# Performance work log

Measured on AMD Instinct MI355X. Metric: run time of the kernel, lower is better.

## Reference

```python
import jax, jax.numpy as jnp
import numpy as np

E = 8       # num experts
D = 768     # embed_dim
H = 12      # num heads
F = 3072    # expert hidden = 4*D
TOPK = 2


def setup_inputs() -> dict:
    key = jax.random.key(0)
    ks = jax.random.split(key, 8)
    B, S = 4, 1024
    s = lambda d: 1.0 / np.sqrt(d)
    return {
        "x": jax.random.normal(ks[0], (B, S, D), jnp.float32),
        "w_qkv": jax.random.normal(ks[1], (D, 3 * D), jnp.float32) * s(D),
        "b_qkv": jnp.zeros((3 * D,), jnp.float32),
        "w_o": jax.random.normal(ks[2], (D, D), jnp.float32) * s(D),
        "b_o": jnp.zeros((D,), jnp.float32),
        "w_router": jax.random.normal(ks[3], (D, E), jnp.float32) * s(D),
        "w1": jax.random.normal(ks[4], (E, D, F), jnp.float32) * s(D),
        "b1": jnp.zeros((E, F), jnp.float32),
        "w2": jax.random.normal(ks[5], (E, F, D), jnp.float32) * s(F),
        "b2": jnp.zeros((E, D), jnp.float32),
    }


def reference(x, w_qkv, b_qkv, w_o, b_o, w_router, w1, b1, w2, b2):
    B, S, Dm = x.shape
    hd = Dm // H
    # --- multi-head self-attention ---
    qkv = x @ w_qkv + b_qkv                                  # [B,S,3D]
    q, k, v = jnp.split(qkv, 3, axis=-1)
    resh = lambda t: t.reshape(B, S, H, hd).transpose(0, 2, 1, 3)  # [B,H,S,hd]
    q, k, v = resh(q), resh(k), resh(v)
    scores = jnp.einsum('bhqd,bhkd->bhqk', q, k) / np.sqrt(hd).astype(np.float32)
    attn = jax.nn.softmax(scores, axis=-1)
    ctx = jnp.einsum('bhqk,bhkd->bhqd', attn, v)
    ctx = ctx.transpose(0, 2, 1, 3).reshape(B, S, Dm)
    y = ctx @ w_o + b_o                                      # [B,S,D]
    # --- top-k MoE feed-forward ---
    t = y.reshape(B * S, Dm)                                 # [T,D]
    logits = t @ w_router                                    # [T,E]
    probs = jax.nn.softmax(logits, axis=-1)
    topv, topi = jax.lax.top_k(probs, TOPK)                  # [T,K]
    topw = topv / jnp.sum(topv, axis=-1, keepdims=True)      # renormalized gates
    T = t.shape[0]
    wfull = jnp.zeros_like(probs).at[jnp.arange(T)[:, None], topi].set(topw)  # [T,E]
    # dense all-expert compute, weighted combine (faithful to routed math)
    h = jax.nn.gelu(jnp.einsum('td,edf->etf', t, w1) + b1[:, None, :])  # [E,T,F]
    oe = jnp.einsum('etf,efd->etd', h, w2) + b2[:, None, :]              # [E,T,D]
    out = jnp.einsum('te,etd->td', wfull, oe).reshape(B, S, Dm)
    diagnostics = probs  # router probabilities as diagnostics
    return (out, diagnostics)
```

## Files before the change

kernel.cpp:

```cpp
#include <hip/hip_runtime.h>
#include <hip/hip_bf16.h>
#include <cstdint>
#include <cmath>

#define T_TOK 4096
#define DIM   768
#define HEADS 12
#define HD    64
#define NEXP  8
#define FDIM  3072

typedef __attribute__((ext_vector_type(8))) short short8v;
typedef __attribute__((ext_vector_type(4))) float float4v;

__device__ __forceinline__ float gelu_tanh(float x) {
  float u = 0.7978845608028654f * (x + 0.044715f * x * x * x);
  return 0.5f * x * (1.0f + tanhf(u));
}

__device__ __forceinline__ short f2bf(float x) {
  __hip_bfloat16 h = __float2bfloat16(x);
  return *reinterpret_cast<short*>(&h);
}

__device__ __forceinline__ void gld16(void* lds, const void* g) {
  __builtin_amdgcn_global_load_lds(
      (__attribute__((address_space(1))) void*)(uintptr_t)g,
      (__attribute__((address_space(3))) void*)(uint32_t)(uintptr_t)lds,
      16, 0, 0);
}

template<int TBM, int TBN, bool BFOUT>
__global__ __launch_bounds__(256) void gemm_f32(
    const float* __restrict__ A, const float* __restrict__ W,
    const float* __restrict__ bias, float* __restrict__ C,
    short* __restrict__ Cbf, int M, int N, int K)
{
  constexpr int MM = TBM / 16;
  constexpr int MN = TBN / 16;
  constexpr int AL4 = TBM / 64;
  constexpr int BL4 = TBN / 64;
  __shared__ float As[16][TBM + 4];
  __shared__ float Bs[16][TBN + 4];
  const int bm = blockIdx.y * TBM;
  const int bn = blockIdx.x * TBN;
  const int tid = threadIdx.x;
  const int tr = tid >> 4;
  const int tc = tid & 15;

  float acc[MM][MN] = {};

  for (int k0 = 0; k0 < K; k0 += 16) {
    #pragma unroll
    for (int i = 0; i < AL4; i++) {
      int fidx = tid + i * 256;
      int row = fidx >> 2, c4 = fidx & 3;
      float4 v = *(const float4*)&A[(size_t)(bm + row) * K + k0 + c4 * 4];
      As[c4 * 4 + 0][row] = v.x;
      As[c4 * 4 + 1][row] = v.y;
      As[c4 * 4 + 2][row] = v.z;
      As[c4 * 4 + 3][row] = v.w;
    }
    #pragma unroll
    for (int i = 0; i < BL4; i++) {
      int fidx = tid + i * 256;
      int kk = fidx / (TBN / 4), n4 = fidx % (TBN / 4);
      *(float4*)&Bs[kk][n4 * 4] =
          *(const float4*)&W[(size_t)(k0 + kk) * N + bn + n4 * 4];
    }
    __syncthreads();
    #pragma unroll
    for (int kk = 0; kk < 16; kk++) {
      float a[MM], b[MN];
      #pragma unroll
      for (int u4 = 0; u4 < MM / 4; u4++) {
        float4 t = *(const float4*)&As[kk][tr * MM + u4 * 4];
        a[u4*4+0]=t.x; a[u4*4+1]=t.y; a[u4*4+2]=t.z; a[u4*4+3]=t.w;
      }
      #pragma unroll
      for (int v4 = 0; v4 < MN / 4; v4++) {
        float4 t = *(const float4*)&Bs[kk][tc * MN + v4 * 4];
        b[v4*4+0]=t.x; b[v4*4+1]=t.y; b[v4*4+2]=t.z; b[v4*4+3]=t.w;
      }
      #pragma unroll
      for (int u = 0; u < MM; u++)
        #pragma unroll
        for (int v = 0; v < MN; v++)
          acc[u][v] = fmaf(a[u], b[v], acc[u][v]);
    }
    __syncthreads();
  }

  #pragma unroll
  for (int u = 0; u < MM; u++) {
    int row = bm + tr * MM + u;
    #pragma unroll
    for (int v4 = 0; v4 < MN / 4; v4++) {
      int col = bn + tc * MN + v4 * 4;
      float4 o;
      o.x = acc[u][v4*4+0] + bias[col+0];
      o.y = acc[u][v4*4+1] + bias[col+1];
      o.z = acc[u][v4*4+2] + bias[col+2];
      o.w = acc[u][v4*4+3] + bias[col+3];
      *(float4*)&C[(size_t)row * N + col] = o;
      if (BFOUT) {
        short4 s = make_short4(f2bf(o.x), f2bf(o.y), f2bf(o.z), f2bf(o.w));
        *(short4*)&Cbf[(size_t)row * N + col] = s;
      }
    }
  }
}

__global__ __launch_bounds__(256) void transpose_bf16(
    const float* __restrict__ W, short* __restrict__ WT, int K, int N)
{
  __shared__ float t[32][33];
  const size_t mat = (size_t)K * N;
  const float* Wp = W + blockIdx.z * mat;
  short* WTp = WT + blockIdx.z * mat;
  int n0 = blockIdx.x * 32, k0 = blockIdx.y * 32;
  int tx = threadIdx.x, ty = threadIdx.y;
  #pragma unroll
  for (int i = 0; i < 4; i++)
    t[ty + i * 8][tx] = Wp[(size_t)(k0 + ty + i * 8) * N + n0 + tx];
  __syncthreads();
  #pragma unroll
  for (int i = 0; i < 4; i++)
    WTp[(size_t)(n0 + ty + i * 8) * K + k0 + tx] = f2bf(t[tx][ty + i * 8]);
}

__global__ __launch_bounds__(256) void moe_up(
    const short* __restrict__ ybf, const short* __restrict__ WT,
    const float* __restrict__ bias, short* __restrict__ hbuf,
    const int* __restrict__ offsets, const int* __restrict__ perm,
    const int* __restrict__ tmap, const int* __restrict__ tilecnt)
{
  const int by = blockIdx.y;
  if (by >= tilecnt[0]) return;
  const int info  = tmap[by];
  const int e     = info >> 16;
  const int start = offsets[e];
  const int M     = offsets[e + 1] - start;
  const int bm    = (info & 0xffff) * 128;
  const int bn    = blockIdx.x * 128;

  __shared__ short As[4][128][8];
  __shared__ short Bs[4][128][8];
  __shared__ int   perm_s[128];

  const int tid  = threadIdx.x;
  const int lane = tid & 63;
  const int wave = tid >> 6;
  const int wm = wave >> 1, wn = wave & 1;
  const int lr = lane & 15;
  const int kb = lane >> 4;

  const short* WTe = WT + (size_t)e * ((size_t)FDIM * DIM);
  const float* be  = bias + (size_t)e * FDIM;

  if (tid < 128) {
    int rr = bm + tid;
    perm_s[tid] = (rr < M) ? perm[start + rr] : perm[start];
  }
  __syncthreads();

  const short* asrc0 = ybf + (size_t)perm_s[lane] * DIM + wave * 8;
  const short* asrc1 = ybf + (size_t)perm_s[64 + lane] * DIM + wave * 8;
  const short* bsrc0 = WTe + (size_t)(bn + lane) * DIM + wave * 8;
  const short* bsrc1 = WTe + (size_t)(bn + 64 + lane) * DIM + wave * 8;
  short* adst0 = &As[wave][0][0];
  short* adst1 = &As[wave][64][0];
  short* bdst0 = &Bs[wave][0][0];
  short* bdst1 = &Bs[wave][64][0];

  float4v acc[4][4] = {};

  for (int k0 = 0; k0 < DIM; k0 += 32) {
    __syncthreads();
    gld16(adst0, asrc0 + k0);
    gld16(adst1, asrc1 + k0);
    gld16(bdst0, bsrc0 + k0);
    gld16(bdst1, bsrc1 + k0);
    __syncthreads();

    short8v af[4], bfv[4];
    #pragma unroll
    for (int mi = 0; mi < 4; mi++)
      af[mi] = *(const short8v*)&As[kb][wm * 64 + mi * 16 + lr][0];
    #pragma unroll
    for (int ni = 0; ni < 4; ni++)
      bfv[ni] = *(const short8v*)&Bs[kb][wn * 64 + ni * 16 + lr][0];
    #pragma unroll
    for (int mi = 0; mi < 4; mi++)
      #pragma unroll
      for (int ni = 0; ni < 4; ni++)
        acc[mi][ni] = __builtin_amdgcn_mfma_f32_16x16x32_bf16(
            af[mi], bfv[ni], acc[mi][ni], 0, 0, 0);
  }

  #pragma unroll
  for (int ni = 0; ni < 4; ni++) {
    int col = bn + wn * 64 + ni * 16 + lr;
    float b = be[col];
    #pragma unroll
    for (int mi = 0; mi < 4; mi++) {
      int lrow0 = wm * 64 + mi * 16 + kb * 4;
      #pragma unroll
      for (int r = 0; r < 4; r++) {
        int rr = bm + lrow0 + r;
        if (rr < M)
          hbuf[(size_t)(start + rr) * FDIM + col] = f2bf(gelu_tanh(acc[mi][ni][r] + b));
      }
    }
  }
}

__global__ __launch_bounds__(256) void moe_down(
    const short* __restrict__ hbuf, const short* __restrict__ WT,
    const float* __restrict__ bias, float* __restrict__ oe,
    const int* __restrict__ offsets,
    const int* __restrict__ tmap, const int* __restrict__ tilecnt)
{
  const int by = blockIdx.y;
  if (by >= tilecnt[1]) return;
  const int info  = tmap[by];
  const int e     = info >> 16;
  const int start = offsets[e];
  const int M     = offsets[e + 1] - start;
  const int bm    = (info & 0xffff) * 64;
  const int bn    = blockIdx.x * 128;

  __shared__ short As[4][64][8];
  __shared__ short Bs[4][128][8];

  const int tid  = threadIdx.x;
  const int lane = tid & 63;
  const int wave = tid >> 6;
  const int lr   = lane & 15;
  const int kb   = lane >> 4;

  const short* WTe = WT + (size_t)e * ((size_t)DIM * FDIM);
  const float* be  = bias + (size_t)e * DIM;

  int arow = bm + lane; if (arow >= M) arow = M - 1;
  const short* asrc  = hbuf + (size_t)(start + arow) * FDIM + wave * 8;
  const short* bsrc0 = WTe + (size_t)(bn + lane) * FDIM + wave * 8;
  const short* bsrc1 = WTe + (size_t)(bn + 64 + lane) * FDIM + wave * 8;
  short* adst  = &As[wave][0][0];
  short* bdst0 = &Bs[wave][0][0];
  short* bdst1 = &Bs[wave][64][0];

  float4v acc[4][2] = {};

  for (int k0 = 0; k0 < FDIM; k0 += 32) {
    __syncthreads();
    gld16(adst,  asrc  + k0);
    gld16(bdst0, bsrc0 + k0);
    gld16(bdst1, bsrc1 + k0);
    __syncthreads();

    short8v af[4], bfv[2];
    #pragma unroll
    for (int mi = 0; mi < 4; mi++)
      af[mi] = *(const short8v*)&As[kb][mi * 16 + lr][0];
    #pragma unroll
    for (int ni = 0; ni < 2; ni++)
      bfv[ni] = *(const short8v*)&Bs[kb][wave * 32 + ni * 16 + lr][0];
    #pragma unroll
    for (int mi = 0; mi < 4; mi++)
      #pragma unroll
      for (int ni = 0; ni < 2; ni++)
        acc[mi][ni] = __builtin_amdgcn_mfma_f32_16x16x32_bf16(
            af[mi], bfv[ni], acc[mi][ni], 0, 0, 0);
  }

  #pragma unroll
  for (int ni = 0; ni < 2; ni++) {
    int col = bn + wave * 32 + ni * 16 + lr;
    float b = be[col];
    #pragma unroll
    for (int mi = 0; mi < 4; mi++) {
      #pragma unroll
      for (int r = 0; r < 4; r++) {
        int rr = bm + mi * 16 + kb * 4 + r;
        if (rr < M)
          oe[(size_t)(start + rr) * DIM + col] = acc[mi][ni][r] + b;
      }
    }
  }
}

__global__ __launch_bounds__(256) void combine_kernel(
    const float* __restrict__ oe, const int* __restrict__ ppos,
    const float* __restrict__ topg, float* __restrict__ out)
{
  int g = blockIdx.x * 256 + threadIdx.x;
  int t = g / 192;
  int c = (g - t * 192) * 4;
  int p0 = ppos[2 * t], p1 = ppos[2 * t + 1];
  float g0 = topg[2 * t], g1 = topg[2 * t + 1];
  float4 a = *(const float4*)&oe[(size_t)p0 * DIM + c];
  float4 b = *(const float4*)&oe[(size_t)p1 * DIM + c];
  float4 o;
  o.x = g0 * a.x + g1 * b.x;
  o.y = g0 * a.y + g1 * b.y;
  o.z = g0 * a.z + g1 * b.z;
  o.w = g0 * a.w + g1 * b.w;
  *(float4*)&out[(size_t)t * DIM + c] = o;
}

__global__ __launch_bounds__(512) void attn_kernel(
    const float* __restrict__ qkv, float* __restrict__ ctx)
{
  const int qt = blockIdx.x;
  const int bh = blockIdx.y;
  const int b = bh / HEADS, h = bh % HEADS;
  const float* base = qkv + (size_t)b * 1024 * (3 * DIM) + h * 64;

  __shared__ float ks[64 * 64];
  __shared__ float vs[64 * 64];
  __shared__ float lred[2][2][32];

  const int tid   = threadIdx.x;
  const int wv    = tid >> 6;
  const int qhalf = wv & 1;
  const int kq    = wv >> 1;
  const int lane  = tid & 63;
  const int grp   = lane >> 2;
  const int sub   = lane & 3;
  const int q0    = qhalf * 32 + grp * 2;
  const int dpart = sub * 16;

  const float qscale = 0.125f * 1.44269504088896f;
  float qA[16], qB[16], accA[16] = {}, accB[16] = {};
  float lA = 0.f, lB = 0.f;

  {
    const float* qpA = base + (size_t)(qt * 64 + q0) * (3 * DIM) + dpart;
    const float* qpB = qpA + 3 * DIM;
    #pragma unroll
    for (int d4 = 0; d4 < 4; d4++) {
      float4 ta = *(const float4*)(qpA + d4 * 4);
      float4 tb = *(const float4*)(qpB + d4 * 4);
      qA[d4*4+0]=ta.x*qscale; qA[d4*4+1]=ta.y*qscale; qA[d4*4+2]=ta.z*qscale; qA[d4*4+3]=ta.w*qscale;
      qB[d4*4+0]=tb.x*qscale; qB[d4*4+1]=tb.y*qscale; qB[d4*4+2]=tb.z*qscale; qB[d4*4+3]=tb.w*qscale;
    }
  }

  for (int kt = 0; kt < 16; kt++) {
    __syncthreads();
    #pragma unroll
    for (int i = 0; i < 2; i++) {
      int idx = tid + i * 512;
      int r = idx >> 4, c4 = idx & 15;
      const float* kp = base + (size_t)(kt * 64 + r) * (3 * DIM) + c4 * 4;
      *(float4*)&ks[r * 64 + c4 * 4] = *(const float4*)(kp + DIM);
      *(float4*)&vs[r * 64 + c4 * 4] = *(const float4*)(kp + 2 * DIM);
    }
    __syncthreads();

    #pragma unroll 2
    for (int jj = 0; jj < 16; jj++) {
      int j = kq * 16 + jj;
      float4 k0v = *(const float4*)&ks[j * 64 + dpart];
      float4 k1v = *(const float4*)&ks[j * 64 + dpart + 4];
      float4 k2v = *(const float4*)&ks[j * 64 + dpart + 8];
      float4 k3v = *(const float4*)&ks[j * 64 + dpart + 12];
      float kr[16] = {k0v.x,k0v.y,k0v.z,k0v.w, k1v.x,k1v.y,k1v.z,k1v.w,
                      k2v.x,k2v.y,k2v.z,k2v.w, k3v.x,k3v.y,k3v.z,k3v.w};
      float sA = 0.f, sB = 0.f;
      #pragma unroll
      for (int d = 0; d < 16; d++) {
        sA = fmaf(qA[d], kr[d], sA);
        sB = fmaf(qB[d], kr[d], sB);
      }
      sA += __shfl_xor(sA, 1);  sB += __shfl_xor(sB, 1);
      sA += __shfl_xor(sA, 2);  sB += __shfl_xor(sB, 2);
      float pA = exp2f(sA);
      float pB = exp2f(sB);
      lA += pA;  lB += pB;
      float4 v0v = *(const float4*)&vs[j * 64 + dpart];
      float4 v1v = *(const float4*)&vs[j * 64 + dpart + 4];
      float4 v2v = *(const float4*)&vs[j * 64 + dpart + 8];
      float4 v3v = *(const float4*)&vs[j * 64 + dpart + 12];
      float vr[16] = {v0v.x,v0v.y,v0v.z,v0v.w, v1v.x,v1v.y,v1v.z,v1v.w,
                      v2v.x,v2v.y,v2v.z,v2v.w, v3v.x,v3v.y,v3v.z,v3v.w};
      #pragma unroll
      for (int d = 0; d < 16; d++) {
        accA[d] = fmaf(pA, vr[d], accA[d]);
        accB[d] = fmaf(pB, vr[d], accB[d]);
      }
    }
  }

  float* regA = ks + qhalf * 2048;
  float* regB = vs + qhalf * 2048;
  const int r0 = (grp * 2) * 64 + dpart;
  const int r1 = r0 + 64;

  __syncthreads();
  if (kq == 2 || kq == 3) {
    float* buf = (kq == 2) ? regA : regB;
    #pragma unroll
    for (int d4 = 0; d4 < 4; d4++) {
      *(float4*)&buf[r0 + d4*4] =
          make_float4(accA[d4*4], accA[d4*4+1], accA[d4*4+2], accA[d4*4+3]);
      *(float4*)&buf[r1 + d4*4] =
          make_float4(accB[d4*4], accB[d4*4+1], accB[d4*4+2], accB[d4*4+3]);
    }
    if (sub == 0) {
      lred[kq - 2][qhalf][grp * 2]     = lA;
      lred[kq - 2][qhalf][grp * 2 + 1] = lB;
    }
  }
  __syncthreads();
  if (kq == 0 || kq == 1) {
    const float* buf = (kq == 0) ? regA : regB;
    #pragma unroll
    for (int d4 = 0; d4 < 4; d4++) {
      float4 a = *(const float4*)&buf[r0 + d4*4];
      float4 c = *(const float4*)&buf[r1 + d4*4];
      accA[d4*4+0] += a.x; accA[d4*4+1] += a.y; accA[d4*4+2] += a.z; accA[d4*4+3] += a.w;
      accB[d4*4+0] += c.x; accB[d4*4+1] += c.y; accB[d4*4+2] += c.z; accB[d4*4+3] += c.w;
    }
    lA += lred[kq][qhalf][grp * 2];
    lB += lred[kq][qhalf][grp * 2 + 1];
  }
  __syncthreads();
  if (kq == 1) {
    #pragma unroll
    for (int d4 = 0; d4 < 4; d4++) {
      *(float4*)&regA[r0 + d4*4] =
          make_float4(accA[d4*4], accA[d4*4+1], accA[d4*4+2], accA[d4*4+3]);
      *(float4*)&regA[r1 + d4*4] =
          make_float4(accB[d4*4], accB[d4*4+1], accB[d4*4+2], accB[d4*4+3]);
    }
    if (sub == 0) {
      lred[0][qhalf][grp * 2]     = lA;
      lred[0][qhalf][grp * 2 + 1] = lB;
    }
  }
  __syncthreads();
  if (kq == 0) {
    #pragma unroll
    for (int d4 = 0; d4 < 4; d4++) {
      float4 a = *(const float4*)&regA[r0 + d4*4];
      float4 c = *(const float4*)&regA[r1 + d4*4];
      accA[d4*4+0] += a.x; accA[d4*4+1] += a.y; accA[d4*4+2] += a.z; accA[d4*4+3] += a.w;
      accB[d4*4+0] += c.x; accB[d4*4+1] += c.y; accB[d4*4+2] += c.z; accB[d4*4+3] += c.w;
    }
    lA += lred[0][qhalf][grp * 2];
    lB += lred[0][qhalf][grp * 2 + 1];
    float invA = 1.f / lA, invB = 1.f / lB;
    float* opA = ctx + ((size_t)b * 1024 + qt * 64 + q0) * DIM + h * 64 + dpart;
    float* opB = opA + DIM;
    #pragma unroll
    for (int d4 = 0; d4 < 4; d4++) {
      float4 oa, ob;
      oa.x = accA[d4*4+0]*invA; oa.y = accA[d4*4+1]*invA;
      oa.z = accA[d4*4+2]*invA; oa.w = accA[d4*4+3]*invA;
      ob.x = accB[d4*4+0]*invB; ob.y = accB[d4*4+1]*invB;
      ob.z = accB[d4*4+2]*invB; ob.w = accB[d4*4+3]*invB;
      *(float4*)(opA + d4 * 4) = oa;
      *(float4*)(opB + d4 * 4) = ob;
    }
  }
}

__global__ __launch_bounds__(256) void router_kernel(
    const float* __restrict__ y, const float* __restrict__ wr,
    float* __restrict__ probs, int* __restrict__ topi,
    float* __restrict__ topg, int* __restrict__ counts)
{
  __shared__ float w[DIM * NEXP];
  const int tid = threadIdx.x;
  for (int i = tid; i < DIM * NEXP; i += 256) w[i] = wr[i];
  __syncthreads();

  const int t = blockIdx.x * 256 + tid;
  const float* yp = y + (size_t)t * DIM;
  float logit[8] = {};
  for (int d = 0; d < DIM; d++) {
    float xv = yp[d];
    #pragma unroll
    for (int e = 0; e < 8; e++) logit[e] = fmaf(xv, w[d * 8 + e], logit[e]);
  }
  float mx = logit[0];
  #pragma unroll
  for (int e = 1; e < 8; e++) mx = fmaxf(mx, logit[e]);
  float p[8], sum = 0.f;
  #pragma unroll
  for (int e = 0; e < 8; e++) { p[e] = __expf(logit[e] - mx); sum += p[e]; }
  float inv = 1.f / sum;
  #pragma unroll
  for (int e = 0; e < 8; e++) { p[e] *= inv; probs[(size_t)t * 8 + e] = p[e]; }

  int i0 = 0;
  #pragma unroll
  for (int e = 1; e < 8; e++) if (p[e] > p[i0]) i0 = e;
  int i1 = (i0 == 0) ? 1 : 0;
  #pragma unroll
  for (int e = 0; e < 8; e++) if (e != i0 && p[e] > p[i1]) i1 = e;
  float g = p[i0] + p[i1];
  topi[2 * t] = i0;  topi[2 * t + 1] = i1;
  topg[2 * t] = p[i0] / g;  topg[2 * t + 1] = p[i1] / g;
  atomicAdd(&counts[i0], 1);
  atomicAdd(&counts[i1], 1);
}

__global__ void init_meta(int* counts) {
  if (threadIdx.x < 8) counts[threadIdx.x] = 0;
}

__global__ void scan_kernel(const int* __restrict__ counts,
                            int* __restrict__ offsets, int* __restrict__ cursors,
                            int* __restrict__ tmap_up, int* __restrict__ tmap_dn,
                            int* __restrict__ tilecnt) {
  if (threadIdx.x == 0) {
    int s = 0;
    for (int e = 0; e < 8; e++) { offsets[e] = s; cursors[e] = s; s += counts[e]; }
    offsets[8] = s;
    int tu = 0, td = 0;
    for (int e = 0; e < 8; e++) {
      int m = counts[e];
      for (int t = 0; t * 128 < m; t++) tmap_up[tu++] = (e << 16) | t;
      for (int t = 0; t * 64  < m; t++) tmap_dn[td++] = (e << 16) | t;
    }
    tilecnt[0] = tu;
    tilecnt[1] = td;
  }
}

__global__ __launch_bounds__(256) void scatter_kernel(
    const int* __restrict__ topi, int* __restrict__ cursors,
    int* __restrict__ perm, int* __restrict__ ppos)
{
  const int t = blockIdx.x * 256 + threadIdx.x;
  #pragma unroll
  for (int s = 0; s < 2; s++) {
    int e = topi[2 * t + s];
    int pos = atomicAdd(&cursors[e], 1);
    perm[pos] = t;
    ppos[2 * t + s] = pos;
  }
}

extern "C" void kernel_launch(void* const* d_in, const int* in_sizes, int n_in,
                              void* d_out, int out_size, void* d_ws, size_t ws_size,
                              hipStream_t stream) {
  const float* x        = (const float*)d_in[0];
  const float* w_qkv    = (const float*)d_in[1];
  const float* b_qkv    = (const float*)d_in[2];
  const float* w_o      = (const float*)d_in[3];
  const float* b_o      = (const float*)d_in[4];
  const float* w_router = (const float*)d_in[5];
  const float* w1       = (const float*)d_in[6];
  const float* b1       = (const float*)d_in[7];
  const float* w2       = (const float*)d_in[8];
  const float* b2       = (const float*)d_in[9];

  float* out   = (float*)d_out;
  float* probs = out + (size_t)T_TOK * DIM;

  char* ws = (char*)d_ws;
  float* qkv  = (float*)ws;
  short* hbuf = (short*)ws;
  short* wT   = (short*)(ws + 50331648);
  float* ctx  = (float*)(ws + 88080384);
  float* oe   = (float*)(ws + 88080384);
  float* y    = (float*)(ws + 100663296);
  short* ybf  = (short*)(ws + 113246208);
  char*  meta = ws + 119537664;
  int*   counts  = (int*)meta;
  int*   cursors = counts + 8;
  int*   offsets = cursors + 8;
  int*   topi    = offsets + 16;
  float* topg    = (float*)(topi + 8192);
  int*   perm    = (int*)(topg + 8192);
  int*   ppos    = perm + 8192;
  int*   tmap_up = ppos + 8192;
  int*   tmap_dn = tmap_up + 80;
  int*   tilecnt = tmap_dn + 144;

  init_meta<<<1, 64, 0, stream>>>(counts);

  gemm_f32<128, 64, false><<<dim3((3 * DIM) / 64, T_TOK / 128), 256, 0, stream>>>(
      x, w_qkv, b_qkv, qkv, nullptr, T_TOK, 3 * DIM, DIM);

  attn_kernel<<<dim3(16, 48), 512, 0, stream>>>(qkv, ctx);

  gemm_f32<64, 64, true><<<dim3(DIM / 64, T_TOK / 64), 256, 0, stream>>>(
      ctx, w_o, b_o, y, ybf, T_TOK, DIM, DIM);

  router_kernel<<<16, 256, 0, stream>>>(y, w_router, probs, topi, topg, counts);
  scan_kernel<<<1, 64, 0, stream>>>(counts, offsets, cursors,
                                    tmap_up, tmap_dn, tilecnt);
  scatter_kernel<<<16, 256, 0, stream>>>(topi, cursors, perm, ppos);

  transpose_bf16<<<dim3(FDIM / 32, DIM / 32, NEXP), dim3(32, 8), 0, stream>>>(
      w1, wT, DIM, FDIM);
  moe_up<<<dim3(FDIM / 128, 72), 256, 0, stream>>>(
      ybf, wT, b1, hbuf, offsets, perm, tmap_up, tilecnt);

  transpose_bf16<<<dim3(DIM / 32, FDIM / 32, NEXP), dim3(32, 8), 0, stream>>>(
      w2, wT, FDIM, DIM);
  moe_down<<<dim3(DIM / 128, 136), 256, 0, stream>>>(
      hbuf, wT, b2, oe, offsets, tmap_dn, tilecnt);

  combine_kernel<<<(T_TOK * DIM / 4) / 256, 256, 0, stream>>>(oe, ppos, topg, out);
}
```

Measured before the change: 1.029 ms.

## Unify MoE up/down GEMMs into templated 128x128 kernel with tile-major grid order

Merges moe_up and moe_down into one templated kernel. The down projection now uses 128x128 tiles with a 4x4 accumulator per wave instead of 64x128, and both launches put the token-tile index on blockIdx.x so consecutive blocks share weight columns. Separately, the attention QK dot product is split into four independent partial sums to shorten the FMA dependency chain. The aim is more reuse per loaded weight tile and more instruction-level parallelism. The cost is fewer blocks for the down GEMM (72x6), which may underfill the GPU's compute units.

Result: faster. 1.005 ms (-2.3%).

```diff
diff --git a/kernel.cpp b/kernel.cpp
--- a/kernel.cpp
+++ b/kernel.cpp
@@ -129,20 +129,22 @@
     WTp[(size_t)(n0 + ty + i * 8) * K + k0 + tx] = f2bf(t[tx][ty + i * 8]);
 }
 
-__global__ __launch_bounds__(256) void moe_up(
-    const short* __restrict__ ybf, const short* __restrict__ WT,
-    const float* __restrict__ bias, short* __restrict__ hbuf,
+template<int MODE>
+__global__ __launch_bounds__(256) void moe_mm(
+    const short* __restrict__ A, const short* __restrict__ WT,
+    const float* __restrict__ bias, void* __restrict__ Cout,
+    int N, int K,
     const int* __restrict__ offsets, const int* __restrict__ perm,
     const int* __restrict__ tmap, const int* __restrict__ tilecnt)
 {
-  const int by = blockIdx.y;
-  if (by >= tilecnt[0]) return;
-  const int info  = tmap[by];
+  const int bx = blockIdx.x;
+  if (bx >= tilecnt[0]) return;
+  const int info  = tmap[bx];
   const int e     = info >> 16;
   const int start = offsets[e];
   const int M     = offsets[e + 1] - start;
   const int bm    = (info & 0xffff) * 128;
-  const int bn    = blockIdx.x * 128;
+  const int bn    = blockIdx.y * 128;
 
   __shared__ short As[4][128][8];
   __shared__ short Bs[4][128][8];
@@ -155,19 +157,30 @@
   const int lr = lane & 15;
   const int kb = lane >> 4;
 
-  const short* WTe = WT + (size_t)e * ((size_t)FDIM * DIM);
-  const float* be  = bias + (size_t)e * FDIM;
-
-  if (tid < 128) {
-    int rr = bm + tid;
-    perm_s[tid] = (rr < M) ? perm[start + rr] : perm[start];
-  }
-  __syncthreads();
-
-  const short* asrc0 = ybf + (size_t)perm_s[lane] * DIM + wave * 8;
-  const short* asrc1 = ybf + (size_t)perm_s[64 + lane] * DIM + wave * 8;
-  const short* bsrc0 = WTe + (size_t)(bn + lane) * DIM + wave * 8;
-  const short* bsrc1 = WTe + (size_t)(bn + 64 + lane) * DIM + wave * 8;
+  const short* WTe = WT + (size_t)e * ((size_t)N * K);
+  const float* be  = bias + (size_t)e * N;
+
+  if (MODE == 1) {
+    if (tid < 128) {
+      int rr = bm + tid;
+      perm_s[tid] = (rr < M) ? perm[start + rr] : perm[start];
+    }
+    __syncthreads();
+  }
+
+  const short* asrc0;
+  const short* asrc1;
+  if (MODE == 1) {
+    asrc0 = A + (size_t)perm_s[lane] * K + wave * 8;
+    asrc1 = A + (size_t)perm_s[64 + lane] * K + wave * 8;
+  } else {
+    int r0 = bm + lane;      if (r0 >= M) r0 = M - 1;
+    int r1 = bm + 64 + lane; if (r1 >= M) r1 = M - 1;
+    asrc0 = A + (size_t)(start + r0) * K + wave * 8;
+    asrc1 = A + (size_t)(start + r1) * K + wave * 8;
+  }
+  const short* bsrc0 = WTe + (size_t)(bn + lane) * K + wave * 8;
+  const short* bsrc1 = WTe + (size_t)(bn + 64 + lane) * K + wave * 8;
   short* adst0 = &As[wave][0][0];
   short* adst1 = &As[wave][64][0];
   short* bdst0 = &Bs[wave][0][0];
@@ -175,7 +188,7 @@
 
   float4v acc[4][4] = {};
 
-  for (int k0 = 0; k0 < DIM; k0 += 32) {
+  for (int k0 = 0; k0 < K; k0 += 32) {
     __syncthreads();
     gld16(adst0, asrc0 + k0);
     gld16(adst1, asrc1 + k0);
@@ -208,83 +221,15 @@
       #pragma unroll
       for (int r = 0; r < 4; r++) {
         int rr = bm + lrow0 + r;
-        if (rr < M)
-          hbuf[(size_t)(start + rr) * FDIM + col] = f2bf(gelu_tanh(acc[mi][ni][r] + b));
-      }
-    }
-  }
-}
-
-__global__ __launch_bounds__(256) void moe_down(
-    const short* __restrict__ hbuf, const short* __restrict__ WT,
-    const float* __restrict__ bias, float* __restrict__ oe,
-    const int* __restrict__ offsets,
-    const int* __restrict__ tmap, const int* __restrict__ tilecnt)
-{
-  const int by = blockIdx.y;
-  if (by >= tilecnt[1]) return;
-  const int info  = tmap[by];
-  const int e     = info >> 16;
-  const int start = offsets[e];
-  const int M     = offsets[e + 1] - start;
-  const int bm    = (info & 0xffff) * 64;
-  const int bn    = blockIdx.x * 128;
-
-  __shared__ short As[4][64][8];
-  __shared__ short Bs[4][128][8];
-
-  const int tid  = threadIdx.x;
-  const int lane = tid & 63;
-  const int wave = tid >> 6;
-  const int lr   = lane & 15;
-  const int kb   = lane >> 4;
-
-  const short* WTe = WT + (size_t)e * ((size_t)DIM * FDIM);
-  const float* be  = bias + (size_t)e * DIM;
-
-  int arow = bm + lane; if (arow >= M) arow = M - 1;
-  const short* asrc  = hbuf + (size_t)(start + arow) * FDIM + wave * 8;
-  const short* bsrc0 = WTe + (size_t)(bn + lane) * FDIM + wave * 8;
-  const short* bsrc1 = WTe + (size_t)(bn + 64 + lane) * FDIM + wave * 8;
-  short* adst  = &As[wave][0][0];
-  short* bdst0 = &Bs[wave][0][0];
-  short* bdst1 = &Bs[wave][64][0];
-
-  float4v acc[4][2] = {};
-
-  for (int k0 = 0; k0 < FDIM; k0 += 32) {
-    __syncthreads();
-    gld16(adst,  asrc  + k0);
-    gld16(bdst0, bsrc0 + k0);
-    gld16(bdst1, bsrc1 + k0);
-    __syncthreads();
-
-    short8v af[4], bfv[2];
-    #pragma unroll
-    for (int mi = 0; mi < 4; mi++)
-      af[mi] = *(const short8v*)&As[kb][mi * 16 + lr][0];
-    #pragma unroll
-    for (int ni = 0; ni < 2; ni++)
-      bfv[ni] = *(const short8v*)&Bs[kb][wave * 32 + ni * 16 + lr][0];
-    #pragma unroll
-    for (int mi = 0; mi < 4; mi++)
-      #pragma unroll
-      for (int ni = 0; ni < 2; ni++)
-        acc[mi][ni] = __builtin_amdgcn_mfma_f32_16x16x32_bf16(
-            af[mi], bfv[ni], acc[mi][ni], 0, 0, 0);
-  }
-
-  #pragma unroll
-  for (int ni = 0; ni < 2; ni++) {
-    int col = bn + wave * 32 + ni * 16 + lr;
-    float b = be[col];
-    #pragma unroll
-    for (int mi = 0; mi < 4; mi++) {
-      #pragma unroll
-      for (int r = 0; r < 4; r++) {
-        int rr = bm + mi * 16 + kb * 4 + r;
-        if (rr < M)
-          oe[(size_t)(start + rr) * DIM + col] = acc[mi][ni][r] + b;
+        if (rr < M) {
+          if (MODE == 1) {
+            short* C = (short*)Cout;
+            C[(size_t)(start + rr) * N + col] = f2bf(gelu_tanh(acc[mi][ni][r] + b));
+          } else {
+            float* C = (float*)Cout;
+            C[(size_t)(start + rr) * N + col] = acc[mi][ni][r] + b;
+          }
+        }
       }
     }
   }
@@ -366,14 +311,25 @@
       float4 k1v = *(const float4*)&ks[j * 64 + dpart + 4];
       float4 k2v = *(const float4*)&ks[j * 64 + dpart + 8];
       float4 k3v = *(const float4*)&ks[j * 64 + dpart + 12];
-      float kr[16] = {k0v.x,k0v.y,k0v.z,k0v.w, k1v.x,k1v.y,k1v.z,k1v.w,
-                      k2v.x,k2v.y,k2v.z,k2v.w, k3v.x,k3v.y,k3v.z,k3v.w};
-      float sA = 0.f, sB = 0.f;
-      #pragma unroll
-      for (int d = 0; d < 16; d++) {
-        sA = fmaf(qA[d], kr[d], sA);
-        sB = fmaf(qB[d], kr[d], sB);
-      }
+      float a0, a1, a2, a3, b0, b1, b2, b3;
+      a0  = qA[0]  * k0v.x; a0 = fmaf(qA[1],  k0v.y, a0);
+      a0  = fmaf(qA[2],  k0v.z, a0); a0 = fmaf(qA[3],  k0v.w, a0);
+      a1  = qA[4]  * k1v.x; a1 = fmaf(qA[5],  k1v.y, a1);
+      a1  = fmaf(qA[6],  k1v.z, a1); a1 = fmaf(qA[7],  k1v.w, a1);
+      a2  = qA[8]  * k2v.x; a2 = fmaf(qA[9],  k2v.y, a2);
+      a2  = fmaf(qA[10], k2v.z, a2); a2 = fmaf(qA[11], k2v.w, a2);
+      a3  = qA[12] * k3v.x; a3 = fmaf(qA[13], k3v.y, a3);
+      a3  = fmaf(qA[14], k3v.z, a3); a3 = fmaf(qA[15], k3v.w, a3);
+      b0  = qB[0]  * k0v.x; b0 = fmaf(qB[1],  k0v.y, b0);
+      b0  = fmaf(qB[2],  k0v.z, b0); b0 = fmaf(qB[3],  k0v.w, b0);
+      b1  = qB[4]  * k1v.x; b1 = fmaf(qB[5],  k1v.y, b1);
+      b1  = fmaf(qB[6],  k1v.z, b1); b1 = fmaf(qB[7],  k1v.w, b1);
+      b2  = qB[8]  * k2v.x; b2 = fmaf(qB[9],  k2v.y, b2);
+      b2  = fmaf(qB[10], k2v.z, b2); b2 = fmaf(qB[11], k2v.w, b2);
+      b3  = qB[12] * k3v.x; b3 = fmaf(qB[13], k3v.y, b3);
+      b3  = fmaf(qB[14], k3v.z, b3); b3 = fmaf(qB[15], k3v.w, b3);
+      float sA = (a0 + a1) + (a2 + a3);
+      float sB = (b0 + b1) + (b2 + b3);
       sA += __shfl_xor(sA, 1);  sB += __shfl_xor(sB, 1);
       sA += __shfl_xor(sA, 2);  sB += __shfl_xor(sB, 2);
       float pA = exp2f(sA);
@@ -514,20 +470,17 @@
 
 __global__ void scan_kernel(const int* __restrict__ counts,
                             int* __restrict__ offsets, int* __restrict__ cursors,
-                            int* __restrict__ tmap_up, int* __restrict__ tmap_dn,
-                            int* __restrict__ tilecnt) {
+                            int* __restrict__ tmap, int* __restrict__ tilecnt) {
   if (threadIdx.x == 0) {
     int s = 0;
     for (int e = 0; e < 8; e++) { offsets[e] = s; cursors[e] = s; s += counts[e]; }
     offsets[8] = s;
-    int tu = 0, td = 0;
+    int tu = 0;
     for (int e = 0; e < 8; e++) {
       int m = counts[e];
-      for (int t = 0; t * 128 < m; t++) tmap_up[tu++] = (e << 16) | t;
-      for (int t = 0; t * 64  < m; t++) tmap_dn[td++] = (e << 16) | t;
+      for (int t = 0; t * 128 < m; t++) tmap[tu++] = (e << 16) | t;
     }
     tilecnt[0] = tu;
-    tilecnt[1] = td;
   }
 }
 
@@ -578,9 +531,8 @@
   float* topg    = (float*)(topi + 8192);
   int*   perm    = (int*)(topg + 8192);
   int*   ppos    = perm + 8192;
-  int*   tmap_up = ppos + 8192;
-  int*   tmap_dn = tmap_up + 80;
-  int*   tilecnt = tmap_dn + 144;
+  int*   tmap    = ppos + 8192;
+  int*   tilecnt = tmap + 80;
 
   init_meta<<<1, 64, 0, stream>>>(counts);
 
@@ -593,19 +545,18 @@
       ctx, w_o, b_o, y, ybf, T_TOK, DIM, DIM);
 
   router_kernel<<<16, 256, 0, stream>>>(y, w_router, probs, topi, topg, counts);
-  scan_kernel<<<1, 64, 0, stream>>>(counts, offsets, cursors,
-                                    tmap_up, tmap_dn, tilecnt);
+  scan_kernel<<<1, 64, 0, stream>>>(counts, offsets, cursors, tmap, tilecnt);
   scatter_kernel<<<16, 256, 0, stream>>>(topi, cursors, perm, ppos);
 
   transpose_bf16<<<dim3(FDIM / 32, DIM / 32, NEXP), dim3(32, 8), 0, stream>>>(
       w1, wT, DIM, FDIM);
-  moe_up<<<dim3(FDIM / 128, 72), 256, 0, stream>>>(
-      ybf, wT, b1, hbuf, offsets, perm, tmap_up, tilecnt);
+  moe_mm<1><<<dim3(72, FDIM / 128), 256, 0, stream>>>(
+      ybf, wT, b1, hbuf, FDIM, DIM, offsets, perm, tmap, tilecnt);
 
   transpose_bf16<<<dim3(DIM / 32, FDIM / 32, NEXP), dim3(32, 8), 0, stream>>>(
       w2, wT, FDIM, DIM);
-  moe_down<<<dim3(DIM / 128, 136), 256, 0, stream>>>(
-      hbuf, wT, b2, oe, offsets, tmap_dn, tilecnt);
+  moe_mm<2><<<dim3(72, DIM / 128), 256, 0, stream>>>(
+      hbuf, wT, b2, oe, DIM, FDIM, offsets, perm, tmap, tilecnt);
 
   combine_kernel<<<(T_TOK * DIM / 4) / 256, 256, 0, stream>>>(oe, ppos, topg, out);
 }
```
